# Kernel optimization log

Hardware: AMD Instinct MI355X
Metric: run time of the kernel (lower is better)

## Reference

```python
import jax, jax.numpy as jnp
import numpy as np

HIDDEN = 4096
N_HEADS = 32
N_KV_HEADS = 8
HEAD_DIM = HIDDEN // N_HEADS  # 128
KV_DIM = N_KV_HEADS * HEAD_DIM  # 1024
ROPE_THETA = 10000.0
B, S = 1, 2048


def setup_inputs() -> dict:
    key = jax.random.key(0)
    ks = jax.random.split(key, 5)
    scale = 0.02
    return {
        "positions": jnp.arange(B * S, dtype=jnp.int32).reshape(B, S),
        "hidden_states": jax.random.normal(ks[0], (B, S, HIDDEN), dtype=jnp.float32),
        "Wqkv": jax.random.normal(ks[1], (HIDDEN, HIDDEN + 2 * KV_DIM), dtype=jnp.float32) * scale,
        "bqkv": jax.random.normal(ks[2], (HIDDEN + 2 * KV_DIM,), dtype=jnp.float32) * scale,
        "Wproj": jax.random.normal(ks[3], (HIDDEN, HIDDEN), dtype=jnp.float32) * scale,
        "bproj": jax.random.normal(ks[4], (HIDDEN,), dtype=jnp.float32) * scale,
    }


def _apply_rope(x, positions):
    # x: [B, S, H, D]; NeoX-style rotation over full head_dim (vLLM get_rope default)
    half = HEAD_DIM // 2
    inv_freq = 1.0 / (ROPE_THETA ** (jnp.arange(0, half, dtype=jnp.float32) / half))
    angles = positions.astype(jnp.float32)[..., None] * inv_freq  # [B, S, half]
    cos = jnp.cos(angles)[:, :, None, :]  # [B, S, 1, half]
    sin = jnp.sin(angles)[:, :, None, :]
    x1, x2 = x[..., :half], x[..., half:]
    return jnp.concatenate([x1 * cos - x2 * sin, x2 * cos + x1 * sin], axis=-1)


def reference(positions, hidden_states, Wqkv, bqkv, Wproj, bproj):
    b, s, _ = hidden_states.shape
    qkv = hidden_states @ Wqkv + bqkv  # [B, S, HIDDEN + 2*KV_DIM]
    q, k, v = jnp.split(qkv, [HIDDEN, HIDDEN + KV_DIM], axis=-1)
    q = q.reshape(b, s, N_HEADS, HEAD_DIM)
    k = k.reshape(b, s, N_KV_HEADS, HEAD_DIM)
    v = v.reshape(b, s, N_KV_HEADS, HEAD_DIM)

    q = _apply_rope(q, positions)
    k = _apply_rope(k, positions)

    # GQA: expand kv heads to query heads (4 query heads per kv head)
    rep = N_HEADS // N_KV_HEADS
    k = jnp.repeat(k, rep, axis=2)  # [B, S, N_HEADS, D]
    v = jnp.repeat(v, rep, axis=2)

    scaling = 1.0 / np.sqrt(HEAD_DIM).astype(np.float32)
    scores = jnp.einsum("bqhd,bkhd->bhqk", q, k) * scaling  # [B, H, S, S]
    causal = jnp.tril(jnp.ones((s, s), dtype=bool))
    scores = jnp.where(causal[None, None], scores, jnp.finfo(scores.dtype).min)
    probs = jax.nn.softmax(scores, axis=-1)
    attn = jnp.einsum("bhqk,bkhd->bqhd", probs, v).reshape(b, s, HIDDEN)

    return attn @ Wproj + bproj
```

## Files before the change

### kernel.cpp

```cpp
#include <hip/hip_runtime.h>

#define HIDDEN 4096
#define NHEADS 32
#define NKV 8
#define HD 128
#define KVD 1024
#define QKVN 6144
#define SEQ 2048

typedef unsigned short u16;
typedef __bf16 bf16x8 __attribute__((ext_vector_type(8)));
typedef float f32x4 __attribute__((ext_vector_type(4)));
typedef unsigned short u16x4 __attribute__((ext_vector_type(4)));

__device__ __forceinline__ u16 f2b(float f) {
  union { float f; unsigned u; } v; v.f = f;
  unsigned r = (v.u + 0x7fffu + ((v.u >> 16) & 1u)) >> 16;
  return (u16)r;
}

__device__ __forceinline__ float b2f(u16 b) {
  union { unsigned u; float f; } v; v.u = ((unsigned)b) << 16;
  return v.f;
}

__device__ __forceinline__ void gl_lds16(const void* g, void* l) {
  __builtin_amdgcn_global_load_lds(
      (const __attribute__((address_space(1))) unsigned*)g,
      (__attribute__((address_space(3))) unsigned*)l, 16, 0, 0);
}

__device__ __forceinline__ f32x4 mfma16(bf16x8 a, bf16x8 b, f32x4 c) {
  return __builtin_amdgcn_mfma_f32_16x16x32_bf16(a, b, c, 0, 0, 0);
}

#define BARRIER() __builtin_amdgcn_s_barrier()
#define WAIT_LGKM0() asm volatile("s_waitcnt lgkmcnt(0)" ::: "memory")
#define WAIT_VM6() asm volatile("s_waitcnt vmcnt(6)" ::: "memory")
#define WAIT_VM0() asm volatile("s_waitcnt vmcnt(0)" ::: "memory")

__global__ void cvt_bf16(const float* __restrict__ x, u16* __restrict__ y, int n) {
  int i = (blockIdx.x * 256 + threadIdx.x) * 4;
  if (i < n) {
    float4 v = *(const float4*)(x + i);
    u16x4 o = {f2b(v.x), f2b(v.y), f2b(v.z), f2b(v.w)};
    *(u16x4*)(y + i) = o;
  }
}

__global__ void transpose_cvt64(const float* __restrict__ W, long ldW,
                                u16* __restrict__ Wt, long ldT) {
  __shared__ float tile[64][65];
  long c0 = blockIdx.x * 64L, r0 = blockIdx.y * 64L;
  int tx = threadIdx.x, ty = threadIdx.y;
#pragma unroll
  for (int i = 0; i < 4; ++i) {
    float4 v = *(const float4*)(W + (r0 + ty + i * 16) * ldW + c0 + tx * 4);
    tile[ty + i * 16][tx * 4 + 0] = v.x;
    tile[ty + i * 16][tx * 4 + 1] = v.y;
    tile[ty + i * 16][tx * 4 + 2] = v.z;
    tile[ty + i * 16][tx * 4 + 3] = v.w;
  }
  __syncthreads();
#pragma unroll
  for (int i = 0; i < 4; ++i) {
    int c = ty + i * 16;
    u16x4 o = {f2b(tile[tx * 4 + 0][c]), f2b(tile[tx * 4 + 1][c]),
               f2b(tile[tx * 4 + 2][c]), f2b(tile[tx * 4 + 3][c])};
    *(u16x4*)(Wt + (c0 + c) * ldT + r0 + tx * 4) = o;
  }
}

__global__ void transpose_b16(const u16* __restrict__ W, long ldW,
                              u16* __restrict__ Wt, long ldT) {
  __shared__ float tile[64][65];
  long c0 = blockIdx.x * 64L, r0 = blockIdx.y * 64L;
  int tx = threadIdx.x, ty = threadIdx.y;
#pragma unroll
  for (int i = 0; i < 4; ++i) {
    u16x4 v = *(const u16x4*)(W + (r0 + ty + i * 16) * ldW + c0 + tx * 4);
    tile[ty + i * 16][tx * 4 + 0] = b2f(v.x);
    tile[ty + i * 16][tx * 4 + 1] = b2f(v.y);
    tile[ty + i * 16][tx * 4 + 2] = b2f(v.z);
    tile[ty + i * 16][tx * 4 + 3] = b2f(v.w);
  }
  __syncthreads();
#pragma unroll
  for (int i = 0; i < 4; ++i) {
    int c = ty + i * 16;
    u16x4 o = {f2b(tile[tx * 4 + 0][c]), f2b(tile[tx * 4 + 1][c]),
               f2b(tile[tx * 4 + 2][c]), f2b(tile[tx * 4 + 3][c])};
    *(u16x4*)(Wt + (c0 + c) * ldT + r0 + tx * 4) = o;
  }
}


#define LOAD_AF(lA, QM)                                                   \
  _Pragma("unroll") for (int mi_ = 0; mi_ < 4; ++mi_) {                   \
    const int ro_ = (wm * 128 + (QM) * 64 + mi_ * 16 + l15) * 64;         \
    af[mi_][0] = *(const bf16x8*)&(lA)[ro_ + sq0];                        \
    af[mi_][1] = *(const bf16x8*)&(lA)[ro_ + sq1];                        \
  }

#define LOAD_BF(lB, QN, DST)                                              \
  _Pragma("unroll") for (int nj_ = 0; nj_ < 2; ++nj_) {                   \
    const int ro_ = (wn * 64 + (QN) * 32 + nj_ * 16 + l15) * 64;          \
    DST[nj_][0] = *(const bf16x8*)&(lB)[ro_ + sq0];                       \
    DST[nj_][1] = *(const bf16x8*)&(lB)[ro_ + sq1];                       \
  }

#define MFMA_BLOCK(MI0, NJ0, BFARR)                                       \
  __builtin_amdgcn_s_setprio(1);                                          \
  _Pragma("unroll") for (int mi_ = 0; mi_ < 4; ++mi_)                     \
  _Pragma("unroll") for (int nj_ = 0; nj_ < 2; ++nj_)                     \
  _Pragma("unroll") for (int ks_ = 0; ks_ < 2; ++ks_)                     \
    acc[(MI0) + mi_][(NJ0) + nj_] =                                       \
        mfma16(af[mi_][ks_], BFARR[nj_][ks_], acc[(MI0) + mi_][(NJ0) + nj_]); \
  __builtin_amdgcn_s_setprio(0);

#define STAGE_A(buf, u, kt)                                               \
  { char* d_ = dA[u] + (buf) * 32768;                                     \
    gl_lds16(aS[u][0] + (long)(kt) * 64, d_);                             \
    gl_lds16(aS[u][1] + (long)(kt) * 64, d_ + 1024); }

#define STAGE_B(buf, u, kt)                                               \
  { char* d_ = dB[u] + (buf) * 32768;                                     \
    gl_lds16(bS[u][0] + (long)(kt) * 64, d_);                             \
    gl_lds16(bS[u][1] + (long)(kt) * 64, d_ + 1024); }

template <bool OUT16>
__global__ __launch_bounds__(512) void gemm256_bt_bias(
    const u16* __restrict__ A, const u16* __restrict__ Bt,
    const float* __restrict__ bias, void* __restrict__ Cv,
    int M, int N, int K) {
  __shared__ u16 As[2][16384];
  __shared__ u16 Bs[2][16384];
  const int t = threadIdx.x;
  const int w = t >> 6, lane = t & 63;
  const int quad = lane >> 4, l15 = lane & 15;
  const int wm = w >> 2, wn = w & 3;
  const long m0 = blockIdx.y * 256L, n0 = blockIdx.x * 256L;
  const int NT = K >> 6;

  const int sq0 = ((quad ^ (l15 & 7)) << 3);
  const int sq1 = sq0 ^ 32;

  const int xs8 = ((lane & 7) ^ (lane >> 3)) * 8;
  const int sr = lane >> 3;
  const u16 *aS[2][2], *bS[2][2];
  char *dA[2], *dB[2];
  {
    const int ra = (w >> 2) * 128 + (w & 3) * 16;
    const int rb = w * 16;
#pragma unroll
    for (int u = 0; u < 2; ++u) {
#pragma unroll
      for (int j = 0; j < 2; ++j) {
        aS[u][j] = A + (m0 + ra + u * 64 + j * 8 + sr) * (long)K + xs8;
        bS[u][j] = Bt + (n0 + rb + u * 128 + j * 8 + sr) * (long)K + xs8;
      }
    }
    dA[0] = (char*)As + ra * 128;
    dA[1] = (char*)As + (ra + 64) * 128;
    dB[0] = (char*)Bs + rb * 128;
    dB[1] = (char*)Bs + (rb + 128) * 128;
  }

  f32x4 acc[8][4] = {};
  bf16x8 af[4][2], bfA[2][2], bfB[2][2];

  STAGE_A(0, 0, 0); STAGE_A(0, 1, 0); STAGE_B(0, 0, 0); STAGE_B(0, 1, 0);
  STAGE_A(1, 0, 1); STAGE_B(1, 0, 1); STAGE_B(1, 1, 1);
  WAIT_VM6();
  BARRIER();

  for (int T = 0; T < NT; T += 2) {
    const bool live = (T + 2 < NT);
    LOAD_AF(As[0], 0);
    LOAD_BF(Bs[0], 0, bfA);
    STAGE_A(1, 1, T + 1);
    BARRIER(); WAIT_LGKM0();
    MFMA_BLOCK(0, 0, bfA);
    BARRIER();
    LOAD_BF(Bs[0], 1, bfB);
    if (live) STAGE_A(0, 0, T + 2);
    BARRIER(); WAIT_LGKM0();
    MFMA_BLOCK(0, 2, bfB);
    BARRIER();
    LOAD_AF(As[0], 1);
    if (live) STAGE_B(0, 0, T + 2);
    BARRIER(); WAIT_LGKM0();
    MFMA_BLOCK(4, 2, bfB);
    BARRIER();
    if (live) { STAGE_B(0, 1, T + 2); WAIT_VM6(); } else { WAIT_VM0(); }
    BARRIER();
    MFMA_BLOCK(4, 0, bfA);
    BARRIER();
    LOAD_AF(As[1], 0);
    LOAD_BF(Bs[1], 0, bfA);
    if (live) STAGE_A(0, 1, T + 2);
    BARRIER(); WAIT_LGKM0();
    MFMA_BLOCK(0, 0, bfA);
    BARRIER();
    LOAD_BF(Bs[1], 1, bfB);
    if (live) STAGE_A(1, 0, T + 3);
    BARRIER(); WAIT_LGKM0();
    MFMA_BLOCK(0, 2, bfB);
    BARRIER();
    LOAD_AF(As[1], 1);
    if (live) STAGE_B(1, 0, T + 3);
    BARRIER(); WAIT_LGKM0();
    MFMA_BLOCK(4, 2, bfB);
    BARRIER();
    if (live) { STAGE_B(1, 1, T + 3); WAIT_VM6(); } else { WAIT_VM0(); }
    BARRIER();
    MFMA_BLOCK(4, 0, bfA);
    BARRIER();
  }

#pragma unroll
  for (int mi = 0; mi < 8; ++mi) {
#pragma unroll
    for (int nj = 0; nj < 4; ++nj) {
      long n = n0 + wn * 64 + nj * 16 + l15;
      float bv = bias[n];
      long mr = m0 + wm * 128 + mi * 16 + quad * 4;
      if constexpr (OUT16) {
        u16* C = (u16*)Cv;
#pragma unroll
        for (int r = 0; r < 4; ++r)
          C[(mr + r) * (long)N + n] = f2b(acc[mi][nj][r] + bv);
      } else {
        float* C = (float*)Cv;
#pragma unroll
        for (int r = 0; r < 4; ++r)
          C[(mr + r) * (long)N + n] = acc[mi][nj][r] + bv;
      }
    }
  }
}

__global__ void rope_qk(const u16* __restrict__ qkv, const int* __restrict__ pos,
                        u16* __restrict__ Qr, u16* __restrict__ Kr) {
  int s = blockIdx.x;
  int hl = threadIdx.x >> 6;
  int d = threadIdx.x & 63;
  int h = blockIdx.y * 4 + hl;
  float p = (float)pos[s];
  float inv = __builtin_amdgcn_exp2f(-(float)d * (13.287712379549449f / 64.0f));
  float ang = p * inv;
  float cs, sn;
  __sincosf(ang, &sn, &cs);
  long base = (long)s * QKVN + (long)h * HD;
  float x1 = b2f(qkv[base + d]), x2 = b2f(qkv[base + d + 64]);
  float o1 = x1 * cs - x2 * sn, o2 = x2 * cs + x1 * sn;
  if (h < NHEADS) {
    const float sc = 0.12751744154f;
    long ob = ((long)h * SEQ + s) * HD;
    Qr[ob + d] = f2b(o1 * sc);
    Qr[ob + d + 64] = f2b(o2 * sc);
  } else {
    long ob = ((long)(h - NHEADS) * SEQ + s) * HD;
    Kr[ob + d] = f2b(o1);
    Kr[ob + d + 64] = f2b(o2);
  }
}

__device__ __forceinline__ void attn_tile(
    const bf16x8 q[4], const u16* KsF, const u16* VsF, u16* Psw,
    bool diag, int wq, int quad, int l15, int sq, f32x4 Oa[8], f32x4& lacc,
    bf16x8 ones) {
  f32x4 s[4] = {};
#pragma unroll
  for (int ks = 0; ks < 4; ++ks) {
#pragma unroll
    for (int nj = 0; nj < 4; ++nj) {
      bf16x8 bk = *reinterpret_cast<const bf16x8*>(
          &KsF[ks * 2048 + (nj * 16 + l15) * 32 + sq * 8]);
      s[nj] = mfma16(q[ks], bk, s[nj]);
    }
  }
#pragma unroll
  for (int nj = 0; nj < 4; ++nj) {
    int key = nj * 16 + l15;
    int ksw = key >> 5, kc = key & 31;
    int khi = kc >> 3, klo = kc & 7;
#pragma unroll
    for (int r = 0; r < 4; ++r) {
      float x = s[nj][r];
      if (diag && key > wq + r) x = -3.0e30f;
      int row = quad * 4 + r;
      Psw[ksw * 512 + row * 32 + ((khi ^ ((row >> 1) & 3)) << 3) + klo] =
          f2b(__builtin_amdgcn_exp2f(x));
    }
  }
#pragma unroll
  for (int ks = 0; ks < 2; ++ks) {
    bf16x8 ap = *reinterpret_cast<const bf16x8*>(&Psw[ks * 512 + l15 * 32 + sq * 8]);
    lacc = mfma16(ap, ones, lacc);
#pragma unroll
    for (int dj = 0; dj < 8; ++dj) {
      bf16x8 bv = *reinterpret_cast<const bf16x8*>(
          &VsF[ks * 4096 + (dj * 16 + l15) * 32 + sq * 8]);
      Oa[dj] = mfma16(ap, bv, Oa[dj]);
    }
  }
}

__global__ __launch_bounds__(256) void attn_fused(
    const u16* __restrict__ Qr, const u16* __restrict__ Kr,
    const u16* __restrict__ Vt, u16* __restrict__ Ao) {
  __shared__ u16 Ks[4 * 64 * 32];
  __shared__ u16 Vs[2 * 128 * 32];
  __shared__ u16 Ps[4][2 * 16 * 32];
  const int px = blockIdx.x, h = blockIdx.y, kvh = h >> 2;
  const int qtA = px, qtB = (SEQ / 64 - 1) - px;
  const int t = threadIdx.x, w = t >> 6, lane = t & 63;
  const int quad = lane >> 4, l15 = lane & 15;
  const int sq = quad ^ ((l15 >> 1) & 3);
  const int wq = w * 16 + quad * 4;
  u16* Psw = &Ps[w][0];

  bf16x8 ones;
  {
    union { u16 u[8]; bf16x8 v; } ou;
#pragma unroll
    for (int i = 0; i < 8; ++i) ou.u[i] = 0x3F80;
    ones = ou.v;
  }

  const long go = (long)(w * 16 + (lane >> 2)) * HD +
                  (long)(((lane & 3) ^ ((lane >> 3) & 3)) * 8);

  bf16x8 qA[4], qB[4];
  {
    const u16* QgA = Qr + ((long)h * SEQ + qtA * 64) * HD;
    const u16* QgB = Qr + ((long)h * SEQ + qtB * 64) * HD;
#pragma unroll
    for (int j = 0; j < 4; ++j) {
      gl_lds16(QgA + go + j * 32, (char*)Ks + j * 4096 + w * 1024);
      gl_lds16(QgB + go + j * 32, (char*)Vs + j * 4096 + w * 1024);
    }
    __syncthreads();
#pragma unroll
    for (int j = 0; j < 4; ++j) {
      qA[j] = *reinterpret_cast<const bf16x8*>(&Ks[j * 2048 + (w * 16 + l15) * 32 + sq * 8]);
      qB[j] = *reinterpret_cast<const bf16x8*>(&Vs[j * 2048 + (w * 16 + l15) * 32 + sq * 8]);
    }
    __syncthreads();
  }

  f32x4 OaA[8] = {}, OaB[8] = {};
  f32x4 lA = {}, lB = {};
  const u16* Kg0 = Kr + (long)kvh * SEQ * HD;
  const u16* Vg0 = Vt + (long)kvh * HD * SEQ;

  for (int kt = 0; kt <= qtB; ++kt) {
    const int k0 = kt * 64;
    {
      const u16* Kg = Kg0 + (long)k0 * HD;
#pragma unroll
      for (int j = 0; j < 4; ++j)
        gl_lds16(Kg + go + j * 32, (char*)Ks + j * 4096 + w * 1024);
      const u16* Vg = Vg0 + k0;
      const int vc = ((lane & 3) ^ ((lane >> 3) & 3)) * 8;
#pragma unroll
      for (int j = 0; j < 4; ++j) {
        int dd = (j & 1) * 64 + w * 16 + (lane >> 2);
        int ks = j >> 1;
        gl_lds16(Vg + (long)dd * SEQ + ks * 32 + vc, (char*)Vs + j * 4096 + w * 1024);
      }
    }
    __syncthreads();

    attn_tile(qB, Ks, Vs, Psw, kt == qtB, wq, quad, l15, sq, OaB, lB, ones);
    if (kt <= qtA)
      attn_tile(qA, Ks, Vs, Psw, kt == qtA, wq, quad, l15, sq, OaA, lA, ones);

    __syncthreads();
  }

#pragma unroll
  for (int r = 0; r < 4; ++r) {
    float invA = 1.0f / lA[r];
    float invB = 1.0f / lB[r];
    long rowA = (long)(qtA * 64 + w * 16 + quad * 4 + r) * HIDDEN + (long)h * HD;
    long rowB = (long)(qtB * 64 + w * 16 + quad * 4 + r) * HIDDEN + (long)h * HD;
#pragma unroll
    for (int dj = 0; dj < 8; ++dj) {
      Ao[rowA + dj * 16 + l15] = f2b(OaA[dj][r] * invA);
      Ao[rowB + dj * 16 + l15] = f2b(OaB[dj][r] * invB);
    }
  }
}

extern "C" void kernel_launch(void* const* d_in, const int* in_sizes, int n_in,
                              void* d_out, int out_size, void* d_ws, size_t ws_size,
                              hipStream_t stream) {
  const int* positions = (const int*)d_in[0];
  const float* hidden = (const float*)d_in[1];
  const float* Wqkv = (const float*)d_in[2];
  const float* bqkv = (const float*)d_in[3];
  const float* Wproj = (const float*)d_in[4];
  const float* bproj = (const float*)d_in[5];
  float* out = (float*)d_out;
  char* ws = (char*)d_ws;

  u16* Wqt = (u16*)(ws);
  u16* Wpt = (u16*)(ws + 50331648L);
  u16* Xb = (u16*)(ws + 83886080L);
  u16* QKVb = (u16*)(ws + 100663296L);
  u16* Qr = (u16*)(ws + 125829120L);
  u16* Kr = (u16*)(ws + 142606336L);
  u16* Vt = (u16*)(ws + 146800640L);
  u16* Ao = (u16*)(ws + 150994944L);

  cvt_bf16<<<8192, 256, 0, stream>>>(hidden, Xb, SEQ * HIDDEN);
  transpose_cvt64<<<dim3(QKVN / 64, HIDDEN / 64), dim3(16, 16), 0, stream>>>(Wqkv, QKVN, Wqt, HIDDEN);
  transpose_cvt64<<<dim3(HIDDEN / 64, HIDDEN / 64), dim3(16, 16), 0, stream>>>(Wproj, HIDDEN, Wpt, HIDDEN);
  gemm256_bt_bias<true><<<dim3(QKVN / 256, SEQ / 256), 512, 0, stream>>>(Xb, Wqt, bqkv, QKVb, SEQ, QKVN, HIDDEN);
  rope_qk<<<dim3(SEQ, 10), 256, 0, stream>>>(QKVb, positions, Qr, Kr);
  transpose_b16<<<dim3(KVD / 64, SEQ / 64), dim3(16, 16), 0, stream>>>(QKVb + 5120, QKVN, Vt, SEQ);
  attn_fused<<<dim3(SEQ / 128, NHEADS), 256, 0, stream>>>(Qr, Kr, Vt, Ao);
  gemm256_bt_bias<false><<<dim3(HIDDEN / 256, SEQ / 256), 512, 0, stream>>>(Ao, Wpt, bproj, out, SEQ, HIDDEN, HIDDEN);
}
```

Before: 583.3 us.

## Software-pipeline LDS fragment loads one MFMA block ahead in GEMM loop

Splits the A-fragment registers into two sets (afL/afH) so each LDS-to-register load is issued one MFMA block ahead of its use. The explicit lgkmcnt(0) waits are removed, leaving the compiler to insert waits just before the MFMAs that consume the data. The goal is to hide LDS read latency behind matrix math in the QKV and output-projection GEMMs. This costs more VGPRs. Some fragment loads now follow the vmcnt wait without an intervening barrier, so they may read LDS before other waves' async copies have landed, which is a correctness risk.

Result: slower. 611.5 us (+4.8%).

```diff
diff --git a/kernel.cpp b/kernel.cpp
--- a/kernel.cpp
+++ b/kernel.cpp
@@ -35,7 +35,6 @@
 }
 
 #define BARRIER() __builtin_amdgcn_s_barrier()
-#define WAIT_LGKM0() asm volatile("s_waitcnt lgkmcnt(0)" ::: "memory")
 #define WAIT_VM6() asm volatile("s_waitcnt vmcnt(6)" ::: "memory")
 #define WAIT_VM0() asm volatile("s_waitcnt vmcnt(0)" ::: "memory")
 
@@ -95,11 +94,11 @@
 }
 
 
-#define LOAD_AF(lA, QM)                                                   \
+#define LOAD_AF(lA, QM, DST)                                              \
   _Pragma("unroll") for (int mi_ = 0; mi_ < 4; ++mi_) {                   \
     const int ro_ = (wm * 128 + (QM) * 64 + mi_ * 16 + l15) * 64;         \
-    af[mi_][0] = *(const bf16x8*)&(lA)[ro_ + sq0];                        \
-    af[mi_][1] = *(const bf16x8*)&(lA)[ro_ + sq1];                        \
+    DST[mi_][0] = *(const bf16x8*)&(lA)[ro_ + sq0];                       \
+    DST[mi_][1] = *(const bf16x8*)&(lA)[ro_ + sq1];                       \
   }
 
 #define LOAD_BF(lB, QN, DST)                                              \
@@ -109,13 +108,13 @@
     DST[nj_][1] = *(const bf16x8*)&(lB)[ro_ + sq1];                       \
   }
 
-#define MFMA_BLOCK(MI0, NJ0, BFARR)                                       \
+#define MFMA_BLOCK(MI0, NJ0, AFARR, BFARR)                                \
   __builtin_amdgcn_s_setprio(1);                                          \
   _Pragma("unroll") for (int mi_ = 0; mi_ < 4; ++mi_)                     \
   _Pragma("unroll") for (int nj_ = 0; nj_ < 2; ++nj_)                     \
   _Pragma("unroll") for (int ks_ = 0; ks_ < 2; ++ks_)                     \
     acc[(MI0) + mi_][(NJ0) + nj_] =                                       \
-        mfma16(af[mi_][ks_], BFARR[nj_][ks_], acc[(MI0) + mi_][(NJ0) + nj_]); \
+        mfma16(AFARR[mi_][ks_], BFARR[nj_][ks_], acc[(MI0) + mi_][(NJ0) + nj_]); \
   __builtin_amdgcn_s_setprio(0);
 
 #define STAGE_A(buf, u, kt)                                               \
@@ -167,54 +166,56 @@
   }
 
   f32x4 acc[8][4] = {};
-  bf16x8 af[4][2], bfA[2][2], bfB[2][2];
+  bf16x8 afL[4][2], afH[4][2], bfA[2][2], bfB[2][2];
 
   STAGE_A(0, 0, 0); STAGE_A(0, 1, 0); STAGE_B(0, 0, 0); STAGE_B(0, 1, 0);
   STAGE_A(1, 0, 1); STAGE_B(1, 0, 1); STAGE_B(1, 1, 1);
   WAIT_VM6();
   BARRIER();
+  LOAD_AF(As[0], 0, afL);
+  LOAD_BF(Bs[0], 0, bfA);
 
   for (int T = 0; T < NT; T += 2) {
     const bool live = (T + 2 < NT);
-    LOAD_AF(As[0], 0);
+    LOAD_BF(Bs[0], 1, bfB);
+    STAGE_A(1, 1, T + 1);
+    BARRIER();
+    MFMA_BLOCK(0, 0, afL, bfA);
+    BARRIER();
+    LOAD_AF(As[0], 1, afH);
+    if (live) STAGE_A(0, 0, T + 2);
+    BARRIER();
+    MFMA_BLOCK(0, 2, afL, bfB);
+    BARRIER();
+    if (live) STAGE_B(0, 0, T + 2);
+    BARRIER();
+    MFMA_BLOCK(4, 0, afH, bfA);
+    BARRIER();
+    if (live) { STAGE_B(0, 1, T + 2); WAIT_VM6(); } else { WAIT_VM0(); }
+    LOAD_AF(As[1], 0, afL);
+    LOAD_BF(Bs[1], 0, bfA);
+    BARRIER();
+    MFMA_BLOCK(4, 2, afH, bfB);
+    BARRIER();
+    LOAD_BF(Bs[1], 1, bfB);
+    if (live) STAGE_A(0, 1, T + 2);
+    BARRIER();
+    MFMA_BLOCK(0, 0, afL, bfA);
+    BARRIER();
+    LOAD_AF(As[1], 1, afH);
+    if (live) STAGE_A(1, 0, T + 3);
+    BARRIER();
+    MFMA_BLOCK(0, 2, afL, bfB);
+    BARRIER();
+    if (live) STAGE_B(1, 0, T + 3);
+    BARRIER();
+    MFMA_BLOCK(4, 0, afH, bfA);
+    BARRIER();
+    if (live) { STAGE_B(1, 1, T + 3); WAIT_VM6(); } else { WAIT_VM0(); }
+    LOAD_AF(As[0], 0, afL);
     LOAD_BF(Bs[0], 0, bfA);
-    STAGE_A(1, 1, T + 1);
-    BARRIER(); WAIT_LGKM0();
-    MFMA_BLOCK(0, 0, bfA);
-    BARRIER();
-    LOAD_BF(Bs[0], 1, bfB);
-    if (live) STAGE_A(0, 0, T + 2);
-    BARRIER(); WAIT_LGKM0();
-    MFMA_BLOCK(0, 2, bfB);
-    BARRIER();
-    LOAD_AF(As[0], 1);
-    if (live) STAGE_B(0, 0, T + 2);
-    BARRIER(); WAIT_LGKM0();
-    MFMA_BLOCK(4, 2, bfB);
-    BARRIER();
-    if (live) { STAGE_B(0, 1, T + 2); WAIT_VM6(); } else { WAIT_VM0(); }
-    BARRIER();
-    MFMA_BLOCK(4, 0, bfA);
-    BARRIER();
-    LOAD_AF(As[1], 0);
-    LOAD_BF(Bs[1], 0, bfA);
-    if (live) STAGE_A(0, 1, T + 2);
-    BARRIER(); WAIT_LGKM0();
-    MFMA_BLOCK(0, 0, bfA);
-    BARRIER();
-    LOAD_BF(Bs[1], 1, bfB);
-    if (live) STAGE_A(1, 0, T + 3);
-    BARRIER(); WAIT_LGKM0();
-    MFMA_BLOCK(0, 2, bfB);
-    BARRIER();
-    LOAD_AF(As[1], 1);
-    if (live) STAGE_B(1, 0, T + 3);
-    BARRIER(); WAIT_LGKM0();
-    MFMA_BLOCK(4, 2, bfB);
-    BARRIER();
-    if (live) { STAGE_B(1, 1, T + 3); WAIT_VM6(); } else { WAIT_VM0(); }
-    BARRIER();
-    MFMA_BLOCK(4, 0, bfA);
+    BARRIER();
+    MFMA_BLOCK(4, 2, afH, bfB);
     BARRIER();
   }
 
```

## Split-K the output projection GEMM and reorder MFMA loop nesting

Applied to the files above, without the earlier changes.

The output projection GEMM now runs as a two-way split-K launch. Its grid grows from 128 to 256 workgroups, which is meant to fill more of the GPU's compute units. Each half writes fp32 partials to separate buffers, and a new elementwise kernel sums them and adds the bias. This costs an extra 32MB partial write/read plus one extra launch. The MFMA block loop is also reordered so the k-slice is outermost, changing instruction interleaving in both GEMMs.

Result: faster. 555.8 us (-4.7%).

```diff
diff --git a/kernel.cpp b/kernel.cpp
--- a/kernel.cpp
+++ b/kernel.cpp
@@ -111,9 +111,9 @@
 
 #define MFMA_BLOCK(MI0, NJ0, BFARR)                                       \
   __builtin_amdgcn_s_setprio(1);                                          \
+  _Pragma("unroll") for (int ks_ = 0; ks_ < 2; ++ks_)                     \
   _Pragma("unroll") for (int mi_ = 0; mi_ < 4; ++mi_)                     \
   _Pragma("unroll") for (int nj_ = 0; nj_ < 2; ++nj_)                     \
-  _Pragma("unroll") for (int ks_ = 0; ks_ < 2; ++ks_)                     \
     acc[(MI0) + mi_][(NJ0) + nj_] =                                       \
         mfma16(af[mi_][ks_], BFARR[nj_][ks_], acc[(MI0) + mi_][(NJ0) + nj_]); \
   __builtin_amdgcn_s_setprio(0);
@@ -128,11 +128,11 @@
     gl_lds16(bS[u][0] + (long)(kt) * 64, d_);                             \
     gl_lds16(bS[u][1] + (long)(kt) * 64, d_ + 1024); }
 
-template <bool OUT16>
+template <int MODE>
 __global__ __launch_bounds__(512) void gemm256_bt_bias(
     const u16* __restrict__ A, const u16* __restrict__ Bt,
-    const float* __restrict__ bias, void* __restrict__ Cv,
-    int M, int N, int K) {
+    const float* __restrict__ bias, void* __restrict__ Cv, void* __restrict__ Cv2,
+    int M, int N, int K, long LDK) {
   __shared__ u16 As[2][16384];
   __shared__ u16 Bs[2][16384];
   const int t = threadIdx.x;
@@ -140,6 +140,7 @@
   const int quad = lane >> 4, l15 = lane & 15;
   const int wm = w >> 2, wn = w & 3;
   const long m0 = blockIdx.y * 256L, n0 = blockIdx.x * 256L;
+  const long kOff = (long)blockIdx.z * K;
   const int NT = K >> 6;
 
   const int sq0 = ((quad ^ (l15 & 7)) << 3);
@@ -156,8 +157,8 @@
     for (int u = 0; u < 2; ++u) {
 #pragma unroll
       for (int j = 0; j < 2; ++j) {
-        aS[u][j] = A + (m0 + ra + u * 64 + j * 8 + sr) * (long)K + xs8;
-        bS[u][j] = Bt + (n0 + rb + u * 128 + j * 8 + sr) * (long)K + xs8;
+        aS[u][j] = A + (m0 + ra + u * 64 + j * 8 + sr) * LDK + kOff + xs8;
+        bS[u][j] = Bt + (n0 + rb + u * 128 + j * 8 + sr) * LDK + kOff + xs8;
       }
     }
     dA[0] = (char*)As + ra * 128;
@@ -223,21 +224,31 @@
 #pragma unroll
     for (int nj = 0; nj < 4; ++nj) {
       long n = n0 + wn * 64 + nj * 16 + l15;
-      float bv = bias[n];
       long mr = m0 + wm * 128 + mi * 16 + quad * 4;
-      if constexpr (OUT16) {
+      if constexpr (MODE == 1) {
+        float bv = bias[n];
         u16* C = (u16*)Cv;
 #pragma unroll
         for (int r = 0; r < 4; ++r)
           C[(mr + r) * (long)N + n] = f2b(acc[mi][nj][r] + bv);
       } else {
-        float* C = (float*)Cv;
+        float* C = blockIdx.z ? (float*)Cv2 : (float*)Cv;
 #pragma unroll
         for (int r = 0; r < 4; ++r)
-          C[(mr + r) * (long)N + n] = acc[mi][nj][r] + bv;
+          C[(mr + r) * (long)N + n] = acc[mi][nj][r];
       }
     }
   }
+}
+
+__global__ void add2_bias(float* __restrict__ o, const float* __restrict__ p1,
+                          const float* __restrict__ bias) {
+  int i = (blockIdx.x * 256 + threadIdx.x) * 4;
+  float4 a = *(float4*)(o + i);
+  float4 b = *(const float4*)(p1 + i);
+  float4 c = *(const float4*)(bias + (i & (HIDDEN - 1)));
+  a.x += b.x + c.x; a.y += b.y + c.y; a.z += b.z + c.z; a.w += b.w + c.w;
+  *(float4*)(o + i) = a;
 }
 
 __global__ void rope_qk(const u16* __restrict__ qkv, const int* __restrict__ pos,
@@ -414,13 +425,17 @@
   u16* Kr = (u16*)(ws + 142606336L);
   u16* Vt = (u16*)(ws + 146800640L);
   u16* Ao = (u16*)(ws + 150994944L);
+  float* P1 = (float*)(ws + 100663296L);
 
   cvt_bf16<<<8192, 256, 0, stream>>>(hidden, Xb, SEQ * HIDDEN);
   transpose_cvt64<<<dim3(QKVN / 64, HIDDEN / 64), dim3(16, 16), 0, stream>>>(Wqkv, QKVN, Wqt, HIDDEN);
   transpose_cvt64<<<dim3(HIDDEN / 64, HIDDEN / 64), dim3(16, 16), 0, stream>>>(Wproj, HIDDEN, Wpt, HIDDEN);
-  gemm256_bt_bias<true><<<dim3(QKVN / 256, SEQ / 256), 512, 0, stream>>>(Xb, Wqt, bqkv, QKVb, SEQ, QKVN, HIDDEN);
+  gemm256_bt_bias<1><<<dim3(QKVN / 256, SEQ / 256), 512, 0, stream>>>(
+      Xb, Wqt, bqkv, QKVb, nullptr, SEQ, QKVN, HIDDEN, HIDDEN);
   rope_qk<<<dim3(SEQ, 10), 256, 0, stream>>>(QKVb, positions, Qr, Kr);
   transpose_b16<<<dim3(KVD / 64, SEQ / 64), dim3(16, 16), 0, stream>>>(QKVb + 5120, QKVN, Vt, SEQ);
   attn_fused<<<dim3(SEQ / 128, NHEADS), 256, 0, stream>>>(Qr, Kr, Vt, Ao);
-  gemm256_bt_bias<false><<<dim3(HIDDEN / 256, SEQ / 256), 512, 0, stream>>>(Ao, Wpt, bproj, out, SEQ, HIDDEN, HIDDEN);
-}
+  gemm256_bt_bias<2><<<dim3(HIDDEN / 256, SEQ / 256, 2), 512, 0, stream>>>(
+      Ao, Wpt, bproj, out, P1, SEQ, HIDDEN, HIDDEN / 2, HIDDEN);
+  add2_bias<<<SEQ * HIDDEN / 1024, 256, 0, stream>>>(out, P1, bproj);
+}
```
